# Optimization experiments

Measured on AMD Instinct MI355X. Metric: run time of the kernel, lower is better.

## Reference

```python
import jax, jax.numpy as jnp
import numpy as np

VOCAB = 100000
EMBED_DIM = 300
TOPK = 10
BATCH = 1024


def setup_inputs() -> dict:
    key = jax.random.key(0)
    k1, k2 = jax.random.split(key)
    wordid = jax.random.randint(k1, (BATCH,), 0, VOCAB, dtype=jnp.int64 if jax.config.jax_enable_x64 else jnp.int32)
    weight = jax.random.normal(k2, (VOCAB, EMBED_DIM), dtype=jnp.float32)
    return {"wordid": wordid, "weight": weight}


def reference(wordid, weight):
    # Embedding lookup: [B, D]
    wordvec = weight[wordid]
    # Dense similarity against full vocab: [B, V]
    sim = jnp.einsum('bd,vd->bv', wordvec, weight)
    # top-(k+1), sorted descending; drop column 0 (the query word itself)
    score, indice = jax.lax.top_k(sim, TOPK + 1)
    return score[:, 1:], indice[:, 1:]
```

## Files before the change

### kernel.cpp

```cpp
#include <hip/hip_runtime.h>
#include <math.h>

#define BATCH 1024
#define VOCAB 100000
#define KDIM  300
#define TOPK  10

#define NKB    10
#define NCB_B  6272
#define NCB_A  64
#define NCC    392
#define NCAND  (NCC*8)
#define NKF    24
#define NDOT   (NKF*4)

typedef __attribute__((ext_vector_type(8))) short bf16x8;
typedef __attribute__((ext_vector_type(4))) float f32x4;
typedef unsigned long long u64;

#define GL2LDS(gsrc, ldst)                                                    \
    __builtin_amdgcn_global_load_lds(                                         \
        (const __attribute__((address_space(1))) void*)(gsrc),                \
        (__attribute__((address_space(3))) void*)(ldst), 16, 0, 0)

__device__ __forceinline__ ushort f2bf(float f) {
    union { float f; unsigned u; } v; v.f = f;
    unsigned r = v.u + 0x7FFFu + ((v.u >> 16) & 1u);
    return (ushort)(r >> 16);
}

__device__ __forceinline__ void ins4(int (&l)[4], int e) {
    if (e <= l[3]) return;
    bool g0 = e > l[0], g1 = e > l[1], g2 = e > l[2];
    l[3] = g2 ? l[2] : e;
    l[2] = g2 ? (g1 ? l[1] : e) : l[2];
    l[1] = g1 ? (g0 ? l[0] : e) : l[1];
    l[0] = g0 ? e : l[0];
}

template<int N>
__device__ __forceinline__ void pins64(u64 (&ks)[N], u64 k) {
    if (k <= ks[N-1]) return;
    #pragma unroll
    for (int p = N-1; p >= 0; --p) {
        bool gt  = k > ks[p];
        bool gtp = (p > 0) ? (k > ks[p-1]) : false;
        ks[p] = gt ? (gtp ? ks[p-1] : k) : ks[p];
    }
}

__global__ __launch_bounds__(256)
void convert_frags(const int* __restrict__ wordid, const float* __restrict__ weight,
                   ushort* __restrict__ ws_b, ushort* __restrict__ ws_a, int nb4)
{
    const int t   = threadIdx.x;
    const int w   = t >> 6, l = t & 63;
    const int bid = blockIdx.x;
    const bool is_a = (bid >= nb4);
    const int cb  = (is_a ? (bid - nb4) : bid) * 4 + w;
    ushort* dst = is_a ? ws_a : ws_b;
    const int kstride = is_a ? 64 : NCB_B;

    const int r16  = l & 15;
    const int ksub = (l >> 4) * 8;

    const int row = is_a ? wordid[cb*16 + r16] : (cb*16 + r16);
    const bool vr = (row < VOCAB);
    const float* src = weight + (size_t)(vr ? row : 0) * KDIM;

    #pragma unroll
    for (int kb = 0; kb < NKB; ++kb) {
        const int k0 = kb*32 + ksub;
        float4 a = make_float4(0.f,0.f,0.f,0.f);
        float4 b = make_float4(0.f,0.f,0.f,0.f);
        if (vr) {
            if (k0 + 8 <= KDIM) {
                a = *reinterpret_cast<const float4*>(src + k0);
                b = *reinterpret_cast<const float4*>(src + k0 + 4);
            } else if (k0 + 4 <= KDIM) {
                a = *reinterpret_cast<const float4*>(src + k0);
            }
        }
        uint4 o;
        o.x = (unsigned)f2bf(a.x) | ((unsigned)f2bf(a.y) << 16);
        o.y = (unsigned)f2bf(a.z) | ((unsigned)f2bf(a.w) << 16);
        o.z = (unsigned)f2bf(b.x) | ((unsigned)f2bf(b.y) << 16);
        o.w = (unsigned)f2bf(b.z) | ((unsigned)f2bf(b.w) << 16);
        *reinterpret_cast<uint4*>(&dst[((size_t)kb*kstride + cb)*512 + (size_t)l*8]) = o;
    }
}

__global__ __launch_bounds__(512, 2)
void sim_gemm(const ushort* __restrict__ ws_a, const ushort* __restrict__ ws_b,
              unsigned* __restrict__ cand)
{
    __shared__ __align__(16) char pool[65536];

    const int id = blockIdx.x;
    const int cc = (id & 7) + ((id >> 5) << 3);
    const int rc = (id >> 3) & 3;

    const int t    = threadIdx.x;
    const int wid  = t >> 6, lane = t & 63;
    const int wm   = wid >> 2, wn = wid & 3;
    const int l16  = lane & 15, lk = lane >> 4;

    auto stageA = [&](int kt, int buf) {
        #pragma unroll
        for (int j = 0; j < 4; ++j) {
            const int slot = wid*4 + j;
            char* ldst = pool + buf*32768 + slot*1024;
            const ushort* src = ws_a
                + ((size_t)(kt*2 + (slot>>4))*64 + rc*16 + (slot & 15))*512
                + (size_t)lane*8;
            GL2LDS(src, (ushort*)ldst);
        }
    };

    auto loadB = [&](int kt, bf16x8 (&b)[2][4]) {
        #pragma unroll
        for (int kb = 0; kb < 2; ++kb)
            #pragma unroll
            for (int nf = 0; nf < 4; ++nf)
                b[kb][nf] = *reinterpret_cast<const bf16x8*>(
                    ws_b + ((size_t)(kt*2 + kb)*NCB_B + cc*16 + wn*4 + nf)*512
                         + (size_t)lane*8);
    };

    f32x4 acc[8][4] = {};
    bf16x8 bA[2][4], bB[2][4];

    stageA(0, 0);
    loadB(0, bA);
    asm volatile("s_waitcnt vmcnt(0)" ::: "memory");
    __builtin_amdgcn_s_barrier();
    asm volatile("" ::: "memory");

    #pragma unroll
    for (int kt = 0; kt < 5; ++kt) {
        const int buf = kt & 1;
        const ushort* Ab = (const ushort*)(pool + buf*32768);
        bf16x8 (&bcur)[2][4] = (kt & 1) ? bB : bA;
        bf16x8 (&bnxt)[2][4] = (kt & 1) ? bA : bB;

        if (kt < 4) {
            stageA(kt + 1, buf ^ 1);
            loadB(kt + 1, bnxt);
        }

        #pragma unroll
        for (int p = 0; p < 4; ++p) {
            bf16x8 af[2][2];
            #pragma unroll
            for (int kb = 0; kb < 2; ++kb)
                #pragma unroll
                for (int m2 = 0; m2 < 2; ++m2)
                    af[kb][m2] = *reinterpret_cast<const bf16x8*>(
                        Ab + (size_t)(kb*16 + wm*8 + p*2 + m2)*512 + lane*8);

            __builtin_amdgcn_s_setprio(1);
            #pragma unroll
            for (int m2 = 0; m2 < 2; ++m2)
                #pragma unroll
                for (int nf = 0; nf < 4; ++nf) {
                    acc[p*2+m2][nf] = __builtin_amdgcn_mfma_f32_16x16x32_bf16(
                        bcur[0][nf], af[0][m2], acc[p*2+m2][nf], 0, 0, 0);
                    acc[p*2+m2][nf] = __builtin_amdgcn_mfma_f32_16x16x32_bf16(
                        bcur[1][nf], af[1][m2], acc[p*2+m2][nf], 0, 0, 0);
                }
            __builtin_amdgcn_s_setprio(0);
        }

        if (kt < 4) {
            asm volatile("s_waitcnt vmcnt(0)" ::: "memory");
            __builtin_amdgcn_s_barrier();
            asm volatile("" ::: "memory");
        }
    }

    __syncthreads();
    int* Cls = (int*)pool;
    #pragma unroll
    for (int mf = 0; mf < 8; ++mf) {
        int k0 = 0, k1 = 0;
        #pragma unroll
        for (int nf = 0; nf < 4; ++nf) {
            float qm = fmaxf(fmaxf(acc[mf][nf][0], acc[mf][nf][1]),
                             fmaxf(acc[mf][nf][2], acc[mf][nf][3]));
            int key = (int)((__float_as_uint(qm) & 0xFFFF0000u)
                            | (unsigned)(wn*16 + nf*4 + lk));
            if (key > k0)      { k1 = k0; k0 = key; }
            else if (key > k1) { k1 = key; }
        }
        int row = wm*128 + mf*16 + l16;
        int ent = wn*4 + lk;
        Cls[row*33 + ent*2 + 0] = k0;
        Cls[row*33 + ent*2 + 1] = k1;
    }
    __syncthreads();

    {
        int row  = t >> 1, half = t & 1;
        int ks[4] = {0, 0, 0, 0};
        #pragma unroll
        for (int j = 0; j < 16; ++j)
            ins4(ks, Cls[row*33 + half*16 + j]);
        int grow = rc*256 + row;
        size_t base = (size_t)grow*NCAND + cc*8 + half*4;
        *reinterpret_cast<uint4*>(&cand[base]) =
            make_uint4((unsigned)ks[0], (unsigned)ks[1],
                       (unsigned)ks[2], (unsigned)ks[3]);
    }
}

__global__ __launch_bounds__(256, 8)
void merge_topq(const unsigned* __restrict__ cand, int* __restrict__ quads)
{
    __shared__ u64 Wv[4*NKF];

    const int row  = blockIdx.x;
    const int t    = threadIdx.x;
    const int wid  = t >> 6, lane = t & 63;

    u64 a[13];
    #pragma unroll
    for (int i = 0; i < 13; ++i) a[i] = 0ull;

    const unsigned* rc = cand + (size_t)row*NCAND;
    #pragma unroll
    for (int i = 0; i < 13; ++i) {
        int off = i*64 + lane;
        if (off < 784) {
            int c = wid*784 + off;
            unsigned e = rc[c];
            u64 comb = ((u64)(e ^ 0x80000000u) << 32)
                     | (unsigned)(((c >> 3) << 6) | (e & 63u));
            pins64<13>(a, comb);
        }
    }

    u64 mywin = 0ull;
    for (int k = 0; k < NKF; ++k) {
        u64 h = a[0], r = h;
        #pragma unroll
        for (int m = 1; m < 64; m <<= 1) {
            u64 o = __shfl_xor(r, m);
            r = (o > r) ? o : r;
        }
        bool win = (h == r);
        #pragma unroll
        for (int j = 0; j < 12; ++j) a[j] = win ? a[j+1] : a[j];
        a[12] = win ? 0ull : a[12];
        mywin = (lane == k) ? r : mywin;
    }
    if (lane < NKF) Wv[wid*NKF + lane] = mywin;
    __syncthreads();

    if (wid == 0) {
        u64 b0 = Wv[lane];
        u64 b1 = (lane < 32) ? Wv[lane + 64] : 0ull;
        if (b1 > b0) { u64 tmp = b0; b0 = b1; b1 = tmp; }

        u64 fin = 0ull;
        for (int k = 0; k < NKF; ++k) {
            u64 h = b0, r = h;
            #pragma unroll
            for (int m = 1; m < 64; m <<= 1) {
                u64 o = __shfl_xor(r, m);
                r = (o > r) ? o : r;
            }
            bool win = (h == r);
            b0 = win ? b1 : b0;
            b1 = win ? 0ull : b1;
            fin = (lane == k) ? r : fin;
        }
        if (lane < NKF) quads[row*NKF + lane] = (int)(fin & 0xffffffffull);
    }
}

__global__ __launch_bounds__(256, 8)
void rescore_exact(const int* __restrict__ quads, const int* __restrict__ wordid,
                   const float* __restrict__ weight, double* __restrict__ scores)
{
    const int g = (blockIdx.x * 256 + threadIdx.x) >> 4;
    const int l = threadIdx.x & 15;
    const int row = g / NDOT;
    const int ci  = g - row * NDOT;

    const int q   = quads[row*NKF + (ci >> 2)];
    const int col = q*4 + (ci & 3);
    const bool valid = (col < VOCAB);
    const int col_eff = valid ? col : 0;

    const float* qr = weight + (size_t)wordid[row]*KDIM;
    const float* wr = weight + (size_t)col_eff*KDIM;

    double a0 = 0.0, a1 = 0.0;
    #pragma unroll
    for (int k = 0; k < 4; ++k) {
        int sl = (l + 16*k) * 4;
        float4 qa = *reinterpret_cast<const float4*>(qr + sl);
        float4 wb = *reinterpret_cast<const float4*>(wr + sl);
        a0 += (double)qa.x * wb.x + (double)qa.z * wb.z;
        a1 += (double)qa.y * wb.y + (double)qa.w * wb.w;
    }
    if (l < 11) {
        int sl = (l + 64) * 4;
        float4 qa = *reinterpret_cast<const float4*>(qr + sl);
        float4 wb = *reinterpret_cast<const float4*>(wr + sl);
        a0 += (double)qa.x * wb.x + (double)qa.z * wb.z;
        a1 += (double)qa.y * wb.y + (double)qa.w * wb.w;
    }
    double a = a0 + a1;
    #pragma unroll
    for (int m = 1; m < 16; m <<= 1) a += __shfl_xor(a, m);

    if (l == 0) scores[g] = valid ? a : -1e300;
}

__global__ __launch_bounds__(64, 8)
void final_select(const double* __restrict__ scores, const int* __restrict__ quads,
                  float* __restrict__ out)
{
    const int row  = blockIdx.x;
    const int lane = threadIdx.x;

    double v0 = -INFINITY, v1 = -INFINITY;
    int    c0 = 0x7fffffff, c1 = 0x7fffffff;
    if (lane < NDOT/2) {
        int i0 = lane*2, i1 = lane*2 + 1;
        v0 = scores[(size_t)row*NDOT + i0];
        v1 = scores[(size_t)row*NDOT + i1];
        c0 = quads[row*NKF + (i0 >> 2)]*4 + (i0 & 3);
        c1 = quads[row*NKF + (i1 >> 2)]*4 + (i1 & 3);
    }

    for (int kk = 0; kk < TOPK + 1; ++kk) {
        bool sel = (v0 > v1) || (v0 == v1 && c0 < c1);
        double bv = sel ? v0 : v1;
        int    bc = sel ? c0 : c1;
        #pragma unroll
        for (int m = 1; m < 64; m <<= 1) {
            double ov = __shfl_xor(bv, m);
            int    oc = __shfl_xor(bc, m);
            if (ov > bv || (ov == bv && oc < bc)) { bv = ov; bc = oc; }
        }
        if (kk >= 1 && lane == 0) {
            out[(size_t)row*TOPK + (kk-1)] = (float)bv;
            out[(size_t)BATCH*TOPK + (size_t)row*TOPK + (kk-1)] = (float)bc;
        }
        if (c0 == bc) v0 = -INFINITY;
        if (c1 == bc) v1 = -INFINITY;
    }
}

extern "C" void kernel_launch(void* const* d_in, const int* in_sizes, int n_in,
                              void* d_out, int out_size, void* d_ws, size_t ws_size,
                              hipStream_t stream) {
    const int*   wordid = (const int*)d_in[0];
    const float* weight = (const float*)d_in[1];
    float* out = (float*)d_out;

    const size_t SZ_B = (size_t)NCB_B * NKB * 64 * 16;
    const size_t SZ_A = (size_t)NCB_A * NKB * 64 * 16;

    char* p = (char*)d_ws;
    ushort*   ws_b = (ushort*)p;  p += SZ_B;
    ushort*   ws_a = (ushort*)p;  p += SZ_A;
    unsigned* cand = (unsigned*)p;

    int*    quads  = (int*)ws_a;
    double* scores = (double*)cand;

    convert_frags<<<NCB_B/4 + NCB_A/4, 256, 0, stream>>>(wordid, weight, ws_b, ws_a, NCB_B/4);
    sim_gemm<<<NCC*4, 512, 0, stream>>>(ws_a, ws_b, cand);
    merge_topq<<<BATCH, 256, 0, stream>>>(cand, quads);
    rescore_exact<<<(BATCH*NDOT)/16, 256, 0, stream>>>(quads, wordid, weight, scores);
    final_select<<<BATCH, 64, 0, stream>>>(scores, quads, out);
}
```

Before: 187.8 us.

## Fuse vocab bf16 conversion into GEMM B-operand loads, drop staging buffer

Removes the separate pass that converted the whole vocabulary matrix to bf16 fragment layout in workspace. The GEMM now reads fp32 rows of the weight matrix directly and converts them to bf16 fragments in registers. This avoids writing and re-reading a roughly 60MB staging buffer. In exchange, the GEMM does twice the global load bytes per B fragment with a less coalesced row-strided pattern, and the B matrix is re-read and re-converted by each of the 4 row-chunk blocks.

```diff
diff --git a/kernel.cpp b/kernel.cpp
--- a/kernel.cpp
+++ b/kernel.cpp
@@ -7,7 +7,6 @@
 #define TOPK  10
 
 #define NKB    10
-#define NCB_B  6272
 #define NCB_A  64
 #define NCC    392
 #define NCAND  (NCC*8)
@@ -50,48 +49,41 @@
 }
 
 __global__ __launch_bounds__(256)
-void convert_frags(const int* __restrict__ wordid, const float* __restrict__ weight,
-                   ushort* __restrict__ ws_b, ushort* __restrict__ ws_a, int nb4)
+void convert_a(const int* __restrict__ wordid, const float* __restrict__ weight,
+               ushort* __restrict__ ws_a)
 {
     const int t   = threadIdx.x;
     const int w   = t >> 6, l = t & 63;
-    const int bid = blockIdx.x;
-    const bool is_a = (bid >= nb4);
-    const int cb  = (is_a ? (bid - nb4) : bid) * 4 + w;
-    ushort* dst = is_a ? ws_a : ws_b;
-    const int kstride = is_a ? 64 : NCB_B;
+    const int cb  = blockIdx.x * 4 + w;
 
     const int r16  = l & 15;
     const int ksub = (l >> 4) * 8;
 
-    const int row = is_a ? wordid[cb*16 + r16] : (cb*16 + r16);
-    const bool vr = (row < VOCAB);
-    const float* src = weight + (size_t)(vr ? row : 0) * KDIM;
+    const int row = wordid[cb*16 + r16];
+    const float* src = weight + (size_t)row * KDIM;
 
     #pragma unroll
     for (int kb = 0; kb < NKB; ++kb) {
         const int k0 = kb*32 + ksub;
         float4 a = make_float4(0.f,0.f,0.f,0.f);
         float4 b = make_float4(0.f,0.f,0.f,0.f);
-        if (vr) {
-            if (k0 + 8 <= KDIM) {
-                a = *reinterpret_cast<const float4*>(src + k0);
-                b = *reinterpret_cast<const float4*>(src + k0 + 4);
-            } else if (k0 + 4 <= KDIM) {
-                a = *reinterpret_cast<const float4*>(src + k0);
-            }
+        if (k0 + 8 <= KDIM) {
+            a = *reinterpret_cast<const float4*>(src + k0);
+            b = *reinterpret_cast<const float4*>(src + k0 + 4);
+        } else if (k0 + 4 <= KDIM) {
+            a = *reinterpret_cast<const float4*>(src + k0);
         }
         uint4 o;
         o.x = (unsigned)f2bf(a.x) | ((unsigned)f2bf(a.y) << 16);
         o.y = (unsigned)f2bf(a.z) | ((unsigned)f2bf(a.w) << 16);
         o.z = (unsigned)f2bf(b.x) | ((unsigned)f2bf(b.y) << 16);
         o.w = (unsigned)f2bf(b.z) | ((unsigned)f2bf(b.w) << 16);
-        *reinterpret_cast<uint4*>(&dst[((size_t)kb*kstride + cb)*512 + (size_t)l*8]) = o;
+        *reinterpret_cast<uint4*>(&ws_a[((size_t)kb*64 + cb)*512 + (size_t)l*8]) = o;
     }
 }
 
 __global__ __launch_bounds__(512, 2)
-void sim_gemm(const ushort* __restrict__ ws_a, const ushort* __restrict__ ws_b,
+void sim_gemm(const ushort* __restrict__ ws_a, const float* __restrict__ weight,
               unsigned* __restrict__ cand)
 {
     __shared__ __align__(16) char pool[65536];
@@ -121,10 +113,27 @@
         #pragma unroll
         for (int kb = 0; kb < 2; ++kb)
             #pragma unroll
-            for (int nf = 0; nf < 4; ++nf)
-                b[kb][nf] = *reinterpret_cast<const bf16x8*>(
-                    ws_b + ((size_t)(kt*2 + kb)*NCB_B + cc*16 + wn*4 + nf)*512
-                         + (size_t)lane*8);
+            for (int nf = 0; nf < 4; ++nf) {
+                const int col = (cc*16 + wn*4 + nf)*16 + l16;
+                const int k0  = (kt*2 + kb)*32 + lk*8;
+                float4 x = make_float4(0.f,0.f,0.f,0.f);
+                float4 y = make_float4(0.f,0.f,0.f,0.f);
+                if (col < VOCAB) {
+                    const float* src = weight + (size_t)col*KDIM + k0;
+                    if (k0 + 8 <= KDIM) {
+                        x = *reinterpret_cast<const float4*>(src);
+                        y = *reinterpret_cast<const float4*>(src + 4);
+                    } else if (k0 + 4 <= KDIM) {
+                        x = *reinterpret_cast<const float4*>(src);
+                    }
+                }
+                uint4 o;
+                o.x = (unsigned)f2bf(x.x) | ((unsigned)f2bf(x.y) << 16);
+                o.y = (unsigned)f2bf(x.z) | ((unsigned)f2bf(x.w) << 16);
+                o.z = (unsigned)f2bf(y.x) | ((unsigned)f2bf(y.y) << 16);
+                o.w = (unsigned)f2bf(y.z) | ((unsigned)f2bf(y.w) << 16);
+                b[kb][nf] = *reinterpret_cast<bf16x8*>(&o);
+            }
     };
 
     f32x4 acc[8][4] = {};
@@ -361,19 +370,17 @@
     const float* weight = (const float*)d_in[1];
     float* out = (float*)d_out;
 
-    const size_t SZ_B = (size_t)NCB_B * NKB * 64 * 16;
     const size_t SZ_A = (size_t)NCB_A * NKB * 64 * 16;
 
     char* p = (char*)d_ws;
-    ushort*   ws_b = (ushort*)p;  p += SZ_B;
     ushort*   ws_a = (ushort*)p;  p += SZ_A;
     unsigned* cand = (unsigned*)p;
 
     int*    quads  = (int*)ws_a;
     double* scores = (double*)cand;
 
-    convert_frags<<<NCB_B/4 + NCB_A/4, 256, 0, stream>>>(wordid, weight, ws_b, ws_a, NCB_B/4);
-    sim_gemm<<<NCC*4, 512, 0, stream>>>(ws_a, ws_b, cand);
+    convert_a<<<NCB_A/4, 256, 0, stream>>>(wordid, weight, ws_a);
+    sim_gemm<<<NCC*4, 512, 0, stream>>>(ws_a, weight, cand);
     merge_topq<<<BATCH, 256, 0, stream>>>(cand, quads);
     rescore_exact<<<(BATCH*NDOT)/16, 256, 0, stream>>>(quads, wordid, weight, scores);
     final_select<<<BATCH, 64, 0, stream>>>(scores, quads, out);
```

New measurement: 343.0 us. 1.83x slower.
